# Optimization experiments

Hardware: AMD Instinct MI355X
Metric: run time of the kernel (lower is better)

The kernel has to match this reference:

```python
import jax, jax.numpy as jnp
import numpy as np
from jax import lax

B, NQ, C = 2, 1024, 2048
H, DH = 16, 128
G, CD = 4, 512          # off_grps, off_dim = C // G
LR, HR = 24, 72         # low-res grid side, high-res grid side
INTER = 64
K = LR * LR             # sampled K/V tokens (grid_size == lr_size)


def setup_inputs() -> dict:
    key = jax.random.key(0)
    ks = jax.random.split(key, 16)
    s = 0.02
    d = {}
    d['hidden_states'] = jax.random.normal(ks[0], (B, NQ, C), jnp.float32)
    d['image_hd'] = jax.random.normal(ks[1], (B, HR * HR, C), jnp.float32)
    d['wq'] = jax.random.normal(ks[2], (C, C), jnp.float32) * s
    d['wk'] = jax.random.normal(ks[3], (C, C), jnp.float32) * s
    d['wv'] = jax.random.normal(ks[4], (C, C), jnp.float32) * s
    d['wo'] = jax.random.normal(ks[5], (C, C), jnp.float32) * s
    d['conv_dw_w'] = jax.random.normal(ks[6], (CD, 1, 3, 3), jnp.float32) * s
    d['ln1_w'] = jnp.ones((CD,), jnp.float32)
    d['ln1_b'] = jnp.zeros((CD,), jnp.float32)
    d['conv_lr_proj_w'] = jax.random.normal(ks[7], (INTER, CD), jnp.float32) * s
    d['proj_int_w'] = jax.random.normal(ks[8], (INTER, CD), jnp.float32) * s
    d['proj_int_b'] = jnp.zeros((INTER,), jnp.float32)
    d['ln2_w'] = jnp.ones((INTER,), jnp.float32)
    d['ln2_b'] = jnp.zeros((INTER,), jnp.float32)
    d['conv_off_w'] = jax.random.normal(ks[9], (2, INTER), jnp.float32) * s
    d['k_hd_w'] = jax.random.normal(ks[10], (C, C), jnp.float32) * s
    d['k_hd_b'] = jnp.zeros((C,), jnp.float32)
    d['v_hd_w'] = jax.random.normal(ks[11], (C, C), jnp.float32) * s
    d['v_hd_b'] = jnp.zeros((C,), jnp.float32)
    return d


def _ln_channels(x, w, b, eps=1e-5):
    # LayerNorm2d: normalize over channel axis of [N, C, H, W]
    mu = jnp.mean(x, axis=1, keepdims=True)
    var = jnp.var(x, axis=1, keepdims=True)
    xn = (x - mu) * lax.rsqrt(var + eps)
    return xn * w[None, :, None, None] + b[None, :, None, None]


def _tokens_to_grid(x, S):
    # [B, S*S, C] -> [B*G, CD, S, S]  (group channels like einops '(b) (h w) (g c) -> (b g) c h w')
    return x.reshape(B, S, S, G, CD).transpose(0, 3, 4, 1, 2).reshape(B * G, CD, S, S)


def _bilinear_sample(img, grid):
    # img [N, C, Hh, Wh]; grid [N, K, 2] (x, y) normalized to [-1, 1], align_corners=True
    N, Cc, Hh, Wh = img.shape
    x = (grid[..., 0] + 1.0) * 0.5 * (Wh - 1)
    y = (grid[..., 1] + 1.0) * 0.5 * (Hh - 1)
    x0f, y0f = jnp.floor(x), jnp.floor(y)
    wx = (x - x0f)[:, None, :]
    wy = (y - y0f)[:, None, :]
    x0 = jnp.clip(x0f.astype(jnp.int32), 0, Wh - 1)
    x1 = jnp.clip(x0 + 1, 0, Wh - 1)
    y0 = jnp.clip(y0f.astype(jnp.int32), 0, Hh - 1)
    y1 = jnp.clip(y0 + 1, 0, Hh - 1)
    imgf = img.reshape(N, Cc, Hh * Wh)
    gather = jax.vmap(lambda im, ix: im[:, ix])  # ([C,HW],[K]) -> [C,K]
    v00 = gather(imgf, y0 * Wh + x0)
    v01 = gather(imgf, y0 * Wh + x1)
    v10 = gather(imgf, y1 * Wh + x0)
    v11 = gather(imgf, y1 * Wh + x1)
    return (v00 * (1 - wx) * (1 - wy) + v01 * wx * (1 - wy)
            + v10 * (1 - wx) * wy + v11 * wx * wy)  # [N, C, K]


def _ref_grid():
    # normalized reference points as in _grid_generate (centers / (S-1) * 2 - 1)
    yy = (jnp.linspace(0.5, LR - 0.5, LR) / (LR - 1.0)) * 2.0 - 1.0
    xx = (jnp.linspace(0.5, LR - 0.5, LR) / (LR - 1.0)) * 2.0 - 1.0
    gy, gx = jnp.meshgrid(yy, xx, indexing='ij')
    return jnp.stack([gx, gy], axis=-1).reshape(K, 2)  # (x, y)


def reference(hidden_states, image_hd, wq, wk, wv, wo, conv_dw_w, ln1_w, ln1_b,
              conv_lr_proj_w, proj_int_w, proj_int_b, ln2_w, ln2_b, conv_off_w,
              k_hd_w, k_hd_b, v_hd_w, v_hd_b):
    # ---- QKV on the full sequence ----
    q = hidden_states @ wq.T
    k_txt = hidden_states @ wk.T
    v_txt = hidden_states @ wv.T

    # ---- offset network on LR image tokens (first LR*LR tokens) ----
    lr = _tokens_to_grid(hidden_states[:, :K, :], LR)          # [B*G, CD, LR, LR]
    x = lax.conv_general_dilated(lr, conv_dw_w, (1, 1), 'SAME',
                                 feature_group_count=CD,
                                 dimension_numbers=('NCHW', 'OIHW', 'NCHW'))
    x = jax.nn.silu(x)
    x = _ln_channels(x, ln1_w, ln1_b)
    x = jnp.einsum('nchw,oc->nohw', x, conv_lr_proj_w)          # 1x1 conv -> [B*G, INTER, LR, LR]
    # intention gate from spatially pooled group features
    pooled = jnp.mean(lr, axis=(2, 3))                          # [B*G, CD]
    gate = jax.nn.sigmoid(pooled @ proj_int_w.T + proj_int_b)   # [B*G, INTER]
    x = x * gate[:, :, None, None]
    x = _ln_channels(x, ln2_w, ln2_b)
    off = jnp.einsum('nchw,oc->nohw', x, conv_off_w)            # [B*G, 2, LR, LR]
    off = off.transpose(0, 2, 3, 1).reshape(B * G, K, 2)        # (x, y)
    pos = jnp.tanh(_ref_grid()[None] + off)                     # sampling locs in [-1, 1]

    # ---- deformable gather from HD features ----
    hd = _tokens_to_grid(image_hd, HR)                          # [B*G, CD, HR, HR]
    samp = _bilinear_sample(hd, pos)                            # [B*G, CD, K]
    samp = samp.reshape(B, G, CD, K).transpose(0, 3, 1, 2).reshape(B, K, C)
    k_hd = samp @ k_hd_w.T + k_hd_b
    v_hd = samp @ v_hd_w.T + v_hd_b

    # ---- attention: causal over text tokens, HD tokens fully visible ----
    k_all = jnp.concatenate([k_txt, k_hd], axis=1)              # [B, NQ+K, C]
    v_all = jnp.concatenate([v_txt, v_hd], axis=1)
    qh = q.reshape(B, NQ, H, DH).transpose(0, 2, 1, 3)
    kh = k_all.reshape(B, NQ + K, H, DH).transpose(0, 2, 1, 3)
    vh = v_all.reshape(B, NQ + K, H, DH).transpose(0, 2, 1, 3)
    scores = jnp.einsum('bhqd,bhkd->bhqk', qh, kh) / jnp.sqrt(jnp.float32(DH))
    col = jnp.arange(NQ + K)
    row = jnp.arange(NQ)
    allow = (col[None, :] >= NQ) | (col[None, :] <= row[:, None])
    scores = jnp.where(allow[None, None], scores, jnp.float32(-1e9))
    attn = jax.nn.softmax(scores, axis=-1)
    out = jnp.einsum('bhqk,bhkd->bhqd', attn, vh)
    out = out.transpose(0, 2, 1, 3).reshape(B, NQ, C)
    return out @ wo.T
```

## Files before the change

### kernel.cpp

```cpp
#include <hip/hip_runtime.h>

typedef unsigned short u16;
typedef unsigned int u32;
typedef __attribute__((ext_vector_type(8))) short bf8;
typedef __attribute__((ext_vector_type(4))) float f4;
typedef __attribute__((ext_vector_type(4))) unsigned short us4;

constexpr int B = 2;
constexpr int NQ = 1024;
constexpr int C = 2048;
constexpr int DH = 128;
constexpr int G = 4;
constexpr int CD = 512;
constexpr int LR = 24;
constexpr int HR = 72;
constexpr int INTER = 64;
constexpr int K = LR * LR;
constexpr int NKV = NQ + K;

#define MFMA16(a, b, c) __builtin_amdgcn_mfma_f32_16x16x32_bf16(a, b, c, 0, 0, 0)
#define GLDS(g, l)                                                         \
  __builtin_amdgcn_global_load_lds(                                        \
      (const __attribute__((address_space(1))) void*)(g),                  \
      (__attribute__((address_space(3))) void*)(l), 16, 0, 0)
#define SB()                               \
  do {                                     \
    __builtin_amdgcn_sched_barrier(0);     \
    __builtin_amdgcn_s_barrier();          \
    __builtin_amdgcn_sched_barrier(0);     \
  } while (0)
#define WVM(n)                                              \
  do {                                                      \
    asm volatile("s_waitcnt vmcnt(" #n ")" ::: "memory");   \
    __builtin_amdgcn_sched_barrier(0);                      \
  } while (0)

__device__ __forceinline__ u16 f2bf1(float f) {
  u32 u = __float_as_uint(f);
  u32 r = (u + 0x7fffu + ((u >> 16) & 1u)) >> 16;
  return (u16)r;
}

__global__ __launch_bounds__(256) void f2bf_direct(
    const float* __restrict__ s0, const float* __restrict__ s1,
    const float* __restrict__ s2, const float* __restrict__ s3,
    const float* __restrict__ s4, const float* __restrict__ s5,
    const float* __restrict__ s6, const float* __restrict__ plrw,
    u16* __restrict__ d0, u16* __restrict__ d1, u16* __restrict__ d2,
    u16* __restrict__ d3, u16* __restrict__ d4, u16* __restrict__ d5,
    u16* __restrict__ d6, float* __restrict__ wt) {
  const int y = blockIdx.y;
  const int t = threadIdx.x;
  if (y == 7) {
    if (blockIdx.x >= 128) return;
    const int idx = blockIdx.x * 256 + t;
    wt[idx] = plrw[(idx & 63) * 512 + (idx >> 6)];
    return;
  }
  const float* s;
  u16* d;
  switch (y) {
    case 0: s = s0; d = d0; break;
    case 1: s = s1; d = d1; break;
    case 2: s = s2; d = d2; break;
    case 3: s = s3; d = d3; break;
    case 4: s = s4; d = d4; break;
    case 5: s = s5; d = d5; break;
    default: s = s6; d = d6; break;
  }
  const int row = t >> 2, c0 = (t & 3) * 16;
  const int fr = row >> 4, rr = row & 15;
  const int colA = c0, colB = c0 + 8;
  const int offA = (((fr * 2 + (colA >> 5)) * 4 + ((colA >> 3) & 3)) * 16 + rr) * 8;
  const int offB = (((fr * 2 + (colB >> 5)) * 4 + ((colB >> 3) & 3)) * 16 + rr) * 8;
#pragma unroll
  for (int p = 0; p < 4; ++p) {
    const int pc = blockIdx.x * 4 + p;
    const int mb = pc >> 5, kb = pc & 31;
    const float* src = s + (size_t)(mb * 64 + row) * 2048 + kb * 64 + c0;
    const float4 v0 = *(const float4*)(src);
    const float4 v1 = *(const float4*)(src + 4);
    const float4 v2 = *(const float4*)(src + 8);
    const float4 v3 = *(const float4*)(src + 12);
    u16* dp = d + (size_t)pc * 4096;
    us4 o0, o1, o2, o3;
    o0.x = f2bf1(v0.x); o0.y = f2bf1(v0.y); o0.z = f2bf1(v0.z); o0.w = f2bf1(v0.w);
    o1.x = f2bf1(v1.x); o1.y = f2bf1(v1.y); o1.z = f2bf1(v1.z); o1.w = f2bf1(v1.w);
    o2.x = f2bf1(v2.x); o2.y = f2bf1(v2.y); o2.z = f2bf1(v2.z); o2.w = f2bf1(v2.w);
    o3.x = f2bf1(v3.x); o3.y = f2bf1(v3.y); o3.z = f2bf1(v3.z); o3.w = f2bf1(v3.w);
    *(us4*)(dp + offA) = o0;
    *(us4*)(dp + offA + 4) = o1;
    *(us4*)(dp + offB) = o2;
    *(us4*)(dp + offB + 4) = o3;
  }
}

__global__ __launch_bounds__(256) void dwpool16(const float* __restrict__ hs,
                                                const float* __restrict__ cdw,
                                                float* __restrict__ x1,
                                                float* __restrict__ pooled) {
  __shared__ float SH[16 * 577];
  const int bidx = blockIdx.x;
  const int n = bidx >> 5, cg = bidx & 31;
  const int b = n >> 2, g = n & 3;
  const int c0 = cg * 16;
  const int t = threadIdx.x;
  {
    const int c = t & 15, pr = t >> 4;
    const float* src = hs + (size_t)b * 1024 * 2048 + g * 512 + c0 + c;
#pragma unroll 4
    for (int j = 0; j < 36; ++j) {
      const int p = j * 16 + pr;
      SH[c * 577 + p] = src[(size_t)p * 2048];
    }
  }
  __syncthreads();
  {
    const int c = t >> 4, seg = t & 15;
    float s = 0.f;
    for (int i = 0; i < 36; ++i) s += SH[c * 577 + seg * 36 + i];
    s += __shfl_xor(s, 1);
    s += __shfl_xor(s, 2);
    s += __shfl_xor(s, 4);
    s += __shfl_xor(s, 8);
    if (seg == 0) pooled[n * 512 + c0 + c] = s * (1.f / 576.f);
  }
  const size_t base_out = (size_t)(n * 512 + c0) * 576;
  for (int j = 0; j < 36; ++j) {
    const int idx = j * 256 + t;
    const int c = idx / 576, p = idx - c * 576;
    const int yy0 = p / 24, xx0 = p - yy0 * 24;
    const float* wp = cdw + (c0 + c) * 9;
    float s = 0.f;
#pragma unroll
    for (int dy = -1; dy <= 1; ++dy)
#pragma unroll
      for (int dx = -1; dx <= 1; ++dx) {
        const int yy = yy0 + dy, xx = xx0 + dx;
        if (yy < 0 || yy >= 24 || xx < 0 || xx >= 24) continue;
        s += SH[c * 577 + yy * 24 + xx] * wp[(dy + 1) * 3 + dx + 1];
      }
    x1[base_out + idx] = s / (1.f + expf(-s));
  }
}

__global__ __launch_bounds__(512, 2) void gemm_queue(
    const u16* __restrict__ Ast, const u16* __restrict__ Wq,
    const u16* __restrict__ Wk, const u16* __restrict__ Wv,
    const u16* __restrict__ sampst, const u16* __restrict__ khwst,
    const u16* __restrict__ vhwst, const float* __restrict__ khb,
    const float* __restrict__ vhb, u16* __restrict__ outq,
    u16* __restrict__ kg, u16* __restrict__ vg, u32* __restrict__ qctr) {
  __shared__ u16 As[2][4][4096];
  __shared__ u16 Bs[2][4][4096];
  __shared__ int s_item;
  const int tid = threadIdx.x, lane = tid & 63, w = tid >> 6;
  const int ks = lane >> 4, r = lane & 15;

  while (true) {
    __syncthreads();
    if (tid == 0) s_item = (int)atomicAdd(qctr, 1u);
    __syncthreads();
    const int item = s_item;
    if (item >= 480) break;

    if (item < 192) {
      const int wm = w >> 2, wn = w & 3;
      const int swz = (item & 7) * 24 + (item >> 3);
      const int mt = swz / 24, nt = swz % 24;
      const u16* Wst = (nt < 8) ? Wq : (nt < 16) ? Wk : Wv;
      const int nb0 = (nt & 7) * 4;
      const int mb0 = mt * 4;

#define ST_A03(bi, kt)                                                        \
  do {                                                                        \
    GLDS(Ast + ((size_t)(mb0 + 0) * 32 + (kt)) * 4096 + tid * 8,              \
         &As[bi][0][tid * 8]);                                                \
    GLDS(Ast + ((size_t)(mb0 + 2) * 32 + (kt)) * 4096 + tid * 8,              \
         &As[bi][2][tid * 8]);                                                \
  } while (0)
#define ST_A47(bi, kt)                                                        \
  do {                                                                        \
    GLDS(Ast + ((size_t)(mb0 + 1) * 32 + (kt)) * 4096 + tid * 8,              \
         &As[bi][1][tid * 8]);                                                \
    GLDS(Ast + ((size_t)(mb0 + 3) * 32 + (kt)) * 4096 + tid * 8,              \
         &As[bi][3][tid * 8]);                                                \
  } while (0)
#define ST_B01(bi, kt)                                                        \
  do {                                                                        \
    GLDS(Wst + ((size_t)(nb0 + 0) * 32 + (kt)) * 4096 + tid * 8,              \
         &Bs[bi][0][tid * 8]);                                                \
    GLDS(Wst + ((size_t)(nb0 + 1) * 32 + (kt)) * 4096 + tid * 8,              \
         &Bs[bi][1][tid * 8]);                                                \
  } while (0)
#define ST_B23(bi, kt)                                                        \
  do {                                                                        \
    GLDS(Wst + ((size_t)(nb0 + 2) * 32 + (kt)) * 4096 + tid * 8,              \
         &Bs[bi][2][tid * 8]);                                                \
    GLDS(Wst + ((size_t)(nb0 + 3) * 32 + (kt)) * 4096 + tid * 8,              \
         &Bs[bi][3][tid * 8]);                                                \
  } while (0)
#define RD_A(dst, bi, half, kc)                                               \
  _Pragma("unroll") for (int i2 = 0; i2 < 4; ++i2) dst[i2] =                  \
      *(const bf8*)(&As[bi][wm * 2 + (half)]                                  \
                       [((i2 * 2 + (kc)) * 4 + ks) * 128 + r * 8]);
#define RD_B(dst, bi, kc)                                                     \
  _Pragma("unroll") for (int j2 = 0; j2 < 4; ++j2) dst[j2] =                  \
      *(const bf8*)(&Bs[bi][wn][((j2 * 2 + (kc)) * 4 + ks) * 128 + r * 8]);
#define MM(ACC, AF, BF)                                                       \
  do {                                                                        \
    __builtin_amdgcn_s_setprio(1);                                            \
    _Pragma("unroll") for (int i3 = 0; i3 < 4; ++i3)                          \
        _Pragma("unroll") for (int j3 = 0; j3 < 4; ++j3) ACC[i3][j3] =        \
            MFMA16(AF[i3], BF[j3], ACC[i3][j3]);                              \
    __builtin_amdgcn_s_setprio(0);                                            \
  } while (0)

      f4 accA[4][4], accB[4][4];
#pragma unroll
      for (int i = 0; i < 4; ++i)
#pragma unroll
        for (int j = 0; j < 4; ++j) {
          accA[i][j] = f4{0.f, 0.f, 0.f, 0.f};
          accB[i][j] = f4{0.f, 0.f, 0.f, 0.f};
        }
      bf8 af[4], b0[4], b1[4];

      ST_A03(0, 0); ST_B01(0, 0); ST_B23(0, 0); ST_A47(0, 0);
      ST_A03(1, 1); ST_B01(1, 1);
      WVM(6);
      SB();

      for (int t = 0; t < 32; ++t) {
        const int buf = t & 1;
        RD_A(af, buf, 0, 0);
        RD_B(b0, buf, 0);
        if (t + 1 < 32) ST_B23(buf ^ 1, t + 1);
        SB();
        MM(accA, af, b0);
        SB();
        RD_A(af, buf, 0, 1);
        RD_B(b1, buf, 1);
        if (t + 1 < 32) ST_A47(buf ^ 1, t + 1);
        SB();
        MM(accA, af, b1);
        if (t + 1 < 32) { WVM(8); } else { WVM(0); }
        SB();
        RD_A(af, buf, 1, 0);
        if (t + 2 < 32) ST_A03(buf, t + 2);
        SB();
        MM(accB, af, b0);
        SB();
        RD_A(af, buf, 1, 1);
        if (t + 2 < 32) ST_B01(buf, t + 2);
        SB();
        MM(accB, af, b1);
        if (t + 2 < 32) { WVM(6); } else if (t + 1 < 32) { WVM(2); }
        SB();
      }

#define EPI(ACC, HALF)                                                        \
  _Pragma("unroll") for (int i = 0; i < 4; ++i)                               \
      _Pragma("unroll") for (int j = 0; j < 4; ++j)                           \
          _Pragma("unroll") for (int rr = 0; rr < 4; ++rr) {                  \
    const int m = mt * 256 + wm * 128 + (HALF)*64 + i * 16 + ks * 4 + rr;     \
    const int n = nt * 256 + wn * 64 + j * 16 + r;                            \
    const float v = ACC[i][j][rr];                                            \
    const int sel = n >> 11, nn = n & 2047, hh = nn >> 7, dd = nn & 127;      \
    const int bb = m >> 10, qq = m & 1023;                                    \
    const u16 bv = f2bf1(v);                                                  \
    if (sel == 0) {                                                           \
      outq[(size_t)m * 2048 + nn] = bv;                                       \
    } else if (sel == 1) {                                                    \
      kg[(((size_t)(bb * 16 + hh) * 50 + (qq >> 5)) * 16 + (dd >> 3)) * 256 + \
         (qq & 31) * 8 + (dd & 7)] = bv;                                      \
    } else {                                                                  \
      vg[((size_t)(bb * 16 + hh) * 200 + (qq >> 3)) * 1024 + dd * 8 +         \
         (qq & 7)] = bv;                                                      \
    }                                                                         \
  }
      EPI(accA, 0)
      EPI(accB, 1)
#undef EPI
    } else {
      u16* A3 = &As[0][0][0];
      u16* B3 = &Bs[0][0][0];
      const int htile = item - 192;
      const bool is_v = (htile >= 144);
      const int hb = is_v ? (htile - 144) : htile;
      const int mt = hb / 16, nt = hb % 16;
      const int ma0 = mt * 2, nb0 = nt * 2;
      const int wr = w >> 2, wc = w & 3;
      const u16* Wsrc = is_v ? vhwst : khwst;

#define HDS1(bi, kt)                                                          \
  do {                                                                        \
    const int kb_ = (kt) >> 1, kc_ = (kt) & 1;                                \
    GLDS(sampst + ((size_t)(ma0 + (w >> 2)) * 32 + kb_) * 4096 +              \
             (w & 3) * 1024 + kc_ * 512 + lane * 8,                           \
         &A3[(bi)*4096 + w * 512 + lane * 8]);                                \
    GLDS(Wsrc + ((size_t)(nb0 + (w >> 2)) * 32 + kb_) * 4096 +                \
             (w & 3) * 1024 + kc_ * 512 + lane * 8,                           \
         &B3[(bi)*4096 + w * 512 + lane * 8]);                                \
  } while (0)

      f4 acc[4][2];
#pragma unroll
      for (int i = 0; i < 4; ++i)
#pragma unroll
        for (int j = 0; j < 2; ++j) acc[i][j] = f4{0.f, 0.f, 0.f, 0.f};

      HDS1(0, 0);
      HDS1(1, 1);
      int rd = 0;
      for (int kt = 0; kt < 64; ++kt) {
        SB();
        if (kt + 2 < 64) {
          const int wb = (rd + 2 >= 3) ? rd - 1 : rd + 2;
          HDS1(wb, kt + 2);
          WVM(4);
        } else if (kt + 1 < 64) {
          WVM(2);
        } else {
          WVM(0);
        }
        SB();
        bf8 af2[4], bw[2];
#pragma unroll
        for (int i = 0; i < 4; ++i)
          af2[i] = *(const bf8*)(&A3[rd * 4096 + (wr * 4 + i) * 512 +
                                     ks * 128 + r * 8]);
#pragma unroll
        for (int j = 0; j < 2; ++j)
          bw[j] = *(const bf8*)(&B3[rd * 4096 + (wc * 2 + j) * 512 +
                                    ks * 128 + r * 8]);
        __builtin_amdgcn_s_setprio(1);
#pragma unroll
        for (int i = 0; i < 4; ++i)
#pragma unroll
          for (int j = 0; j < 2; ++j)
            acc[i][j] = MFMA16(af2[i], bw[j], acc[i][j]);
        __builtin_amdgcn_s_setprio(0);
        rd = (rd + 1 >= 3) ? 0 : rd + 1;
      }
#undef HDS1
      const int rbase = ks * 4;
      const float* bias = is_v ? vhb : khb;
#pragma unroll
      for (int i = 0; i < 4; ++i)
#pragma unroll
        for (int j = 0; j < 2; ++j) {
          const int nn = nt * 128 + (wc * 2 + j) * 16 + r;
          const int hh = nn >> 7, dd = nn & 127;
#pragma unroll
          for (int rr = 0; rr < 4; ++rr) {
            const int m = mt * 128 + wr * 64 + i * 16 + rbase + rr;
            const int bb = m / 576;
            const int kv = 1024 + (m - bb * 576);
            const u16 bv = f2bf1(acc[i][j][rr] + bias[nn]);
            if (!is_v) {
              kg[(((size_t)(bb * 16 + hh) * 50 + (kv >> 5)) * 16 + (dd >> 3)) *
                     256 +
                 (kv & 31) * 8 + (dd & 7)] = bv;
            } else {
              vg[((size_t)(bb * 16 + hh) * 200 + (kv >> 3)) * 1024 + dd * 8 +
                 (kv & 7)] = bv;
            }
          }
        }
    }
  }
}

__global__ __launch_bounds__(256) void gemm_out3(const u16* __restrict__ Ast,
                                                 const u16* __restrict__ W0,
                                                 float* __restrict__ outf) {
  __shared__ u16 As[3][4096];
  __shared__ u16 Bs[3][4096];
  const int tid = threadIdx.x, lane = tid & 63, w = tid >> 6;
  const int wr = w >> 1, wc = w & 1;
  const int ksl = lane >> 4, rl = lane & 15;
  const int xcd = blockIdx.x & 7, idx = blockIdx.x >> 3;
  const int mt = (xcd >> 2) * 8 + idx / 4;
  const int nt = (xcd & 3) * 4 + idx % 4;
  const u16* Wp = W0;
  const int ma0 = mt * 2;
  const int nb0 = nt * 2;

#define GST2(dstArr, srcBase, tb0, kt)                                     \
  do {                                                                     \
    const int kb_ = (kt) >> 1, kc_ = (kt) & 1;                             \
    _Pragma("unroll") for (int r2 = 0; r2 < 2; ++r2) {                     \
      const int run = r2 * 4 + w;                                          \
      GLDS(srcBase + ((size_t)((tb0) + (run >> 2)) * 32 + kb_) * 4096 +    \
               (run & 3) * 1024 + kc_ * 512 + lane * 8,                    \
           &dstArr[run * 512 + lane * 8]);                                 \
    }                                                                      \
  } while (0)

  f4 acc[4][4];
#pragma unroll
  for (int i = 0; i < 4; ++i)
#pragma unroll
    for (int j = 0; j < 4; ++j) acc[i][j] = f4{0.f, 0.f, 0.f, 0.f};

  GST2(As[0], Ast, ma0, 0);
  GST2(Bs[0], Wp, nb0, 0);
  GST2(As[1], Ast, ma0, 1);
  GST2(Bs[1], Wp, nb0, 1);
  int rd = 0;
  for (int kt = 0; kt < 64; ++kt) {
    SB();
    if (kt + 2 < 64) {
      const int wb = (rd + 2 >= 3) ? rd - 1 : rd + 2;
      GST2(As[wb], Ast, ma0, kt + 2);
      GST2(Bs[wb], Wp, nb0, kt + 2);
      WVM(8);
    } else if (kt + 1 < 64) {
      WVM(4);
    } else {
      WVM(0);
    }
    SB();
    bf8 af[4], bw[4];
#pragma unroll
    for (int i = 0; i < 4; ++i)
      af[i] = *(const bf8*)(&As[rd][(wr * 4 + i) * 512 + ksl * 128 + rl * 8]);
#pragma unroll
    for (int j = 0; j < 4; ++j)
      bw[j] = *(const bf8*)(&Bs[rd][(wc * 4 + j) * 512 + ksl * 128 + rl * 8]);
    __builtin_amdgcn_s_setprio(1);
#pragma unroll
    for (int i = 0; i < 4; ++i)
#pragma unroll
      for (int j = 0; j < 4; ++j)
        acc[i][j] = MFMA16(af[i], bw[j], acc[i][j]);
    __builtin_amdgcn_s_setprio(0);
    rd = (rd + 1 >= 3) ? 0 : rd + 1;
  }
#undef GST2

  const int rbase = ksl * 4;
#pragma unroll
  for (int i = 0; i < 4; ++i)
#pragma unroll
    for (int j = 0; j < 4; ++j) {
      const int n = nt * 128 + wc * 64 + j * 16 + rl;
#pragma unroll
      for (int rr = 0; rr < 4; ++rr) {
        const int m = mt * 128 + wr * 64 + i * 16 + rbase + rr;
        outf[(size_t)m * 2048 + n] = acc[i][j][rr];
      }
    }
}

__global__ __launch_bounds__(256) void lnproj_gate(
    const float* __restrict__ x1, const float* __restrict__ ln1w,
    const float* __restrict__ ln1b, const float* __restrict__ wt,
    const float* __restrict__ pooled, const float* __restrict__ piw,
    const float* __restrict__ pib, float* __restrict__ x2,
    float* __restrict__ gate) {
  __shared__ float Xs[512][68];
  __shared__ float rs[4][64], rss[4][64];
  const int bidx = blockIdx.x;
  const int t = threadIdx.x;
  if (bidx >= 72) {
    const int idx = (bidx - 72) * 256 + t;
    const int n = idx >> 6, o = idx & 63;
    const float* pb = pooled + n * 512;
    const float* wb = piw + o * 512;
    float s = pib[o];
    for (int c = 0; c < 512; ++c) s += pb[c] * wb[c];
    gate[idx] = 1.f / (1.f + expf(-s));
    return;
  }
  const int n = bidx / 9, pc = bidx % 9;
  const int p0 = pc * 64;
  {
    const int pl = t & 63, c4 = t >> 6;
    const float* src = x1 + (size_t)n * 512 * 576 + p0 + pl;
#pragma unroll 4
    for (int j = 0; j < 128; ++j) {
      const int c = j * 4 + c4;
      Xs[c][pl] = src[(size_t)c * 576];
    }
  }
  __syncthreads();
  {
    const int pl = t & 63, q = t >> 6;
    float s = 0.f, ss = 0.f;
    for (int c = q * 128; c < q * 128 + 128; ++c) {
      const float v = Xs[c][pl];
      s += v;
      ss += v * v;
    }
    rs[q][pl] = s;
    rss[q][pl] = ss;
    __syncthreads();
    const float S = rs[0][pl] + rs[1][pl] + rs[2][pl] + rs[3][pl];
    const float SS = rss[0][pl] + rss[1][pl] + rss[2][pl] + rss[3][pl];
    const float mean = S * (1.f / 512.f);
    const float inv = rsqrtf(SS * (1.f / 512.f) - mean * mean + 1e-5f);
    for (int c = q * 128; c < q * 128 + 128; ++c)
      Xs[c][pl] = (Xs[c][pl] - mean) * inv * ln1w[c] + ln1b[c];
  }
  __syncthreads();
  {
    const int o4 = (t & 15) * 4, pl0 = (t >> 4) * 4;
    float acc[4][4] = {};
    for (int c = 0; c < 512; ++c) {
      const f4 xv = *(const f4*)(&Xs[c][pl0]);
      const f4 wv = *(const f4*)(&wt[c * 64 + o4]);
#pragma unroll
      for (int i = 0; i < 4; ++i)
#pragma unroll
        for (int j = 0; j < 4; ++j) acc[i][j] += wv[i] * xv[j];
    }
#pragma unroll
    for (int i = 0; i < 4; ++i) {
      f4 ov;
      ov[0] = acc[i][0]; ov[1] = acc[i][1];
      ov[2] = acc[i][2]; ov[3] = acc[i][3];
      *(f4*)(&x2[(size_t)(n * 64 + o4 + i) * 576 + p0 + pl0]) = ov;
    }
  }
}

__global__ __launch_bounds__(256) void pos_sample(
    const float* __restrict__ x2, const float* __restrict__ gate,
    const float* __restrict__ ln2w, const float* __restrict__ ln2b,
    const float* __restrict__ offw, const float* __restrict__ img,
    u16* __restrict__ sampst) {
  const int bk = blockIdx.x;
  const int b = bk / K, k = bk % K;
  __shared__ int s_idx[G][4];
  __shared__ float s_w[G][4];
  const int t = threadIdx.x;
  const int g = t >> 6, lane = t & 63;
  {
    const int n = b * G + g;
    float v = x2[((size_t)n * INTER + lane) * K + k] * gate[n * INTER + lane];
    float s = v, ss = v * v;
    for (int o = 32; o; o >>= 1) {
      s += __shfl_xor(s, o);
      ss += __shfl_xor(ss, o);
    }
    const float mean = s * (1.f / INTER);
    const float var = ss * (1.f / INTER) - mean * mean;
    const float xn = (v - mean) * rsqrtf(var + 1e-5f) * ln2w[lane] + ln2b[lane];
    float ox = xn * offw[lane];
    float oy = xn * offw[INTER + lane];
    for (int o = 32; o; o >>= 1) {
      ox += __shfl_xor(ox, o);
      oy += __shfl_xor(oy, o);
    }
    if (lane == 0) {
      const int yi = k / LR, xi = k % LR;
      const float rx = (xi + 0.5f) / 23.f * 2.f - 1.f;
      const float ry = (yi + 0.5f) / 23.f * 2.f - 1.f;
      const float px = tanhf(rx + ox), py = tanhf(ry + oy);
      const float x = (px + 1.f) * 0.5f * (HR - 1);
      const float y = (py + 1.f) * 0.5f * (HR - 1);
      const float x0f = floorf(x), y0f = floorf(y);
      const float wx = x - x0f, wy = y - y0f;
      const int x0 = min(max((int)x0f, 0), HR - 1);
      const int x1 = min(x0 + 1, HR - 1);
      const int y0 = min(max((int)y0f, 0), HR - 1);
      const int y1 = min(y0 + 1, HR - 1);
      s_idx[g][0] = y0 * HR + x0;
      s_idx[g][1] = y0 * HR + x1;
      s_idx[g][2] = y1 * HR + x0;
      s_idx[g][3] = y1 * HR + x1;
      s_w[g][0] = (1.f - wx) * (1.f - wy);
      s_w[g][1] = wx * (1.f - wy);
      s_w[g][2] = (1.f - wx) * wy;
      s_w[g][3] = wx * wy;
    }
  }
  __syncthreads();
  const int m = b * 576 + k;
  const int mb = m >> 6, fr = (m >> 4) & 3, r = m & 15;
  const int ch0 = t * 8;
  const int gg = ch0 >> 9;
  const float* ib = img + (size_t)b * HR * HR * C + ch0;
  float v[8];
#pragma unroll
  for (int j = 0; j < 8; ++j) v[j] = 0.f;
#pragma unroll
  for (int q = 0; q < 4; ++q) {
    const float wq_ = s_w[gg][q];
    const float* p = ib + (size_t)s_idx[gg][q] * C;
    const float4 a = *(const float4*)p;
    const float4 c = *(const float4*)(p + 4);
    v[0] += wq_ * a.x; v[1] += wq_ * a.y; v[2] += wq_ * a.z; v[3] += wq_ * a.w;
    v[4] += wq_ * c.x; v[5] += wq_ * c.y; v[6] += wq_ * c.z; v[7] += wq_ * c.w;
  }
  const int kb = ch0 >> 6, kc = (ch0 >> 5) & 1, ks3 = (ch0 >> 3) & 3;
  u16* dst = sampst + ((size_t)(mb * 32 + kb)) * 4096 +
             (((fr * 2 + kc) * 4 + ks3) * 16 + r) * 8;
  us4 o0, o1;
  o0.x = f2bf1(v[0]); o0.y = f2bf1(v[1]); o0.z = f2bf1(v[2]); o0.w = f2bf1(v[3]);
  o1.x = f2bf1(v[4]); o1.y = f2bf1(v[5]); o1.z = f2bf1(v[6]); o1.w = f2bf1(v[7]);
  *(us4*)dst = o0;
  *(us4*)(dst + 4) = o1;
}

__global__ __launch_bounds__(256) void attn_u64(
    const u16* __restrict__ qb, const u16* __restrict__ kg,
    const u16* __restrict__ vg, u16* __restrict__ aob_st) {
  const int i = blockIdx.x;
  const int pair = i & 255, half = i >> 8;
  const int bh = pair & 31;
  const int q8 = pair >> 5;
  const int qblk = half ? (15 - q8) : q8;
  const int b = bh >> 4, h = bh & 15;
  const int q0 = qblk * 64;
  const int tid = threadIdx.x, lane = tid & 63, w = tid >> 6;
  const int qw = q0 + w * 16;
  const int col = lane & 15, kpart = lane >> 4, rbase = kpart * 4;
  __shared__ u16 Ks[2][8192];
  __shared__ u16 Vs[2][8192];
  __shared__ u16 Pl[4][16 * 72];
  bf8 qf[4];
  {
    const u16* qp =
        qb + (size_t)(b * 1024 + qw + col) * 2048 + h * 128 + kpart * 8;
#pragma unroll
    for (int dc = 0; dc < 4; ++dc) qf[dc] = *(const bf8*)(qp + dc * 32);
  }
  f4 o[8];
#pragma unroll
  for (int df = 0; df < 8; ++df) o[df] = f4{0.f, 0.f, 0.f, 0.f};
  float m_r[4] = {-1e30f, -1e30f, -1e30f, -1e30f};
  float l_p[4] = {0.f, 0.f, 0.f, 0.f};
  const float scale = 0.08838834764831845f;
  const int nt_text = qblk + 1;
  const int nt = nt_text + 9;
  const u16* kbh = kg + (size_t)bh * (NKV * 128);
  const u16* vbh = vg + (size_t)bh * (NKV * 128);
  u16* pw = &Pl[w][0];

#define ASTG64(bi, kv0)                                                       \
  do {                                                                        \
    const u16* gk = kbh + (size_t)((kv0) >> 5) * 4096 + w * 2048 + lane * 8;  \
    GLDS(gk, &Ks[bi][w * 2048 + lane * 8]);                                   \
    GLDS(gk + 512, &Ks[bi][w * 2048 + 512 + lane * 8]);                       \
    GLDS(gk + 1024, &Ks[bi][w * 2048 + 1024 + lane * 8]);                     \
    GLDS(gk + 1536, &Ks[bi][w * 2048 + 1536 + lane * 8]);                     \
    const u16* gv = vbh + (size_t)((kv0) >> 3) * 1024 + w * 2048 + lane * 8;  \
    GLDS(gv, &Vs[bi][w * 2048 + lane * 8]);                                   \
    GLDS(gv + 512, &Vs[bi][w * 2048 + 512 + lane * 8]);                       \
    GLDS(gv + 1024, &Vs[bi][w * 2048 + 1024 + lane * 8]);                     \
    GLDS(gv + 1536, &Vs[bi][w * 2048 + 1536 + lane * 8]);                     \
  } while (0)

  ASTG64(0, 0);
  int cur = 0;
  for (int t = 0; t < nt; ++t) {
    const bool is_text = t < nt_text;
    const int kv0 = is_text ? (t << 6) : (1024 + ((t - nt_text) << 6));
    SB();
    if (t + 1 < nt) {
      const int t1 = t + 1;
      const int kv1 =
          (t1 < nt_text) ? (t1 << 6) : (1024 + ((t1 - nt_text) << 6));
      ASTG64(cur ^ 1, kv1);
      WVM(8);
    } else {
      WVM(0);
    }
    SB();
    const u16* ksb = &Ks[cur][0];
    const u16* vsb = &Vs[cur][0];
    f4 s0 = {0.f, 0.f, 0.f, 0.f}, s1 = {0.f, 0.f, 0.f, 0.f};
    f4 s2 = {0.f, 0.f, 0.f, 0.f}, s3 = {0.f, 0.f, 0.f, 0.f};
    __builtin_amdgcn_s_setprio(1);
#pragma unroll
    for (int dc = 0; dc < 4; ++dc) {
      const int dblk = dc * 4 + kpart;
      bf8 k0f = *(const bf8*)(ksb + (dblk * 32 + col) * 8);
      bf8 k1f = *(const bf8*)(ksb + (dblk * 32 + 16 + col) * 8);
      bf8 k2f = *(const bf8*)(ksb + 4096 + (dblk * 32 + col) * 8);
      bf8 k3f = *(const bf8*)(ksb + 4096 + (dblk * 32 + 16 + col) * 8);
      s0 = MFMA16(qf[dc], k0f, s0);
      s1 = MFMA16(qf[dc], k1f, s1);
      s2 = MFMA16(qf[dc], k2f, s2);
      s3 = MFMA16(qf[dc], k3f, s3);
    }
    __builtin_amdgcn_s_setprio(0);
    float sa[4][4], loc[4], p[4][4];
    bool grow = false;
    const bool need_mask = is_text && (kv0 + 63 > qw);
#pragma unroll
    for (int rr = 0; rr < 4; ++rr) {
      float a0 = s0[rr] * scale, a1 = s1[rr] * scale;
      float a2 = s2[rr] * scale, a3 = s3[rr] * scale;
      if (need_mask) {
        const int qg = qw + rbase + rr;
        if (kv0 + col > qg) a0 = -1e30f;
        if (kv0 + 16 + col > qg) a1 = -1e30f;
        if (kv0 + 32 + col > qg) a2 = -1e30f;
        if (kv0 + 48 + col > qg) a3 = -1e30f;
      }
      sa[rr][0] = a0; sa[rr][1] = a1; sa[rr][2] = a2; sa[rr][3] = a3;
      loc[rr] = fmaxf(fmaxf(a0, a1), fmaxf(a2, a3));
      grow |= (loc[rr] > m_r[rr] + 8.f);
    }
    if (__any(grow)) {
      float fr[4];
#pragma unroll
      for (int rr = 0; rr < 4; ++rr) {
        float mx = loc[rr];
        mx = fmaxf(mx, __shfl_xor(mx, 1));
        mx = fmaxf(mx, __shfl_xor(mx, 2));
        mx = fmaxf(mx, __shfl_xor(mx, 4));
        mx = fmaxf(mx, __shfl_xor(mx, 8));
        const float mn = fmaxf(m_r[rr], mx);
        fr[rr] = __expf(m_r[rr] - mn);
        m_r[rr] = mn;
#pragma unroll
        for (int jj = 0; jj < 4; ++jj) p[rr][jj] = __expf(sa[rr][jj] - mn);
        l_p[rr] = l_p[rr] * fr[rr] + p[rr][0] + p[rr][1] + p[rr][2] + p[rr][3];
      }
#pragma unroll
      for (int df = 0; df < 8; ++df) {
        o[df][0] *= fr[0]; o[df][1] *= fr[1];
        o[df][2] *= fr[2]; o[df][3] *= fr[3];
      }
    } else {
#pragma unroll
      for (int rr = 0; rr < 4; ++rr) {
#pragma unroll
        for (int jj = 0; jj < 4; ++jj) p[rr][jj] = __expf(sa[rr][jj] - m_r[rr]);
        l_p[rr] += p[rr][0] + p[rr][1] + p[rr][2] + p[rr][3];
      }
    }
#pragma unroll
    for (int rr = 0; rr < 4; ++rr) {
      pw[(rbase + rr) * 72 + col] = f2bf1(p[rr][0]);
      pw[(rbase + rr) * 72 + 16 + col] = f2bf1(p[rr][1]);
      pw[(rbase + rr) * 72 + 32 + col] = f2bf1(p[rr][2]);
      pw[(rbase + rr) * 72 + 48 + col] = f2bf1(p[rr][3]);
    }
    bf8 pa0 = *(const bf8*)(pw + col * 72 + kpart * 8);
    bf8 pa1 = *(const bf8*)(pw + col * 72 + 32 + kpart * 8);
    __builtin_amdgcn_s_setprio(1);
#pragma unroll
    for (int df = 0; df < 8; ++df) {
      bf8 vf0 = *(const bf8*)(vsb + (kpart * 128 + df * 16 + col) * 8);
      bf8 vf1 = *(const bf8*)(vsb + ((kpart + 4) * 128 + df * 16 + col) * 8);
      o[df] = MFMA16(pa0, vf0, o[df]);
      o[df] = MFMA16(pa1, vf1, o[df]);
    }
    __builtin_amdgcn_s_setprio(0);
    cur ^= 1;
  }
#undef ASTG64
  float inv[4];
#pragma unroll
  for (int rr = 0; rr < 4; ++rr) {
    float ps = l_p[rr];
    ps += __shfl_xor(ps, 1);
    ps += __shfl_xor(ps, 2);
    ps += __shfl_xor(ps, 4);
    ps += __shfl_xor(ps, 8);
    inv[rr] = 1.f / ps;
  }
#pragma unroll
  for (int rr = 0; rr < 4; ++rr) {
    const int m = b * 1024 + qw + rbase + rr;
    const int mb = m >> 6, fr3 = (m >> 4) & 3, r16 = m & 15;
#pragma unroll
    for (int df = 0; df < 8; ++df) {
      const int ncol = h * 128 + df * 16 + col;
      const int kb = ncol >> 6, kc = (ncol >> 5) & 1, ks3 = (ncol >> 3) & 3,
                j0 = ncol & 7;
      aob_st[((size_t)(mb * 32 + kb)) * 4096 +
             (((fr3 * 2 + kc) * 4 + ks3) * 16 + r16) * 8 + j0] =
          f2bf1(o[df][rr] * inv[rr]);
    }
  }
}

extern "C" void kernel_launch(void* const* d_in, const int* in_sizes, int n_in,
                              void* d_out, int out_size, void* d_ws,
                              size_t ws_size, hipStream_t stream) {
  const float* hs = (const float*)d_in[0];
  const float* img = (const float*)d_in[1];
  const float* wq = (const float*)d_in[2];
  const float* wk = (const float*)d_in[3];
  const float* wv = (const float*)d_in[4];
  const float* wo = (const float*)d_in[5];
  const float* cdw = (const float*)d_in[6];
  const float* ln1w = (const float*)d_in[7];
  const float* ln1b = (const float*)d_in[8];
  const float* plrw = (const float*)d_in[9];
  const float* piw = (const float*)d_in[10];
  const float* pib = (const float*)d_in[11];
  const float* ln2w = (const float*)d_in[12];
  const float* ln2b = (const float*)d_in[13];
  const float* offw = (const float*)d_in[14];
  const float* khw = (const float*)d_in[15];
  const float* khb = (const float*)d_in[16];
  const float* vhw = (const float*)d_in[17];
  const float* vhb = (const float*)d_in[18];
  float* outp = (float*)d_out;

  u16* wsp = (u16*)d_ws;
  const size_t SZ = 4194304;
  u16* hs_st = wsp;
  u16* wq_st = wsp + SZ;
  u16* wk_st = wsp + 2 * SZ;
  u16* wv_st = wsp + 3 * SZ;
  u16* wo_st = wsp + 4 * SZ;
  u16* khw_st = wsp + 5 * SZ;
  u16* vhw_st = wsp + 6 * SZ;
  u16* qb_bf = wsp + 7 * SZ;
  u16* samp_st = wsp + 8 * SZ;
  u16* kg = wsp + 8 * SZ + 2359296;
  u16* vg = kg + 6553600;
  float* x1b = (float*)kg + 2359296;
  float* x2b = x1b + 2359296;
  float* poolb = x2b + 294912;
  float* gb = poolb + 4096;
  float* wtb = (float*)(vg + 6553600);
  u32* qctr = (u32*)(wtb + 32768);
  u16* aob_st = wq_st;

  dim3 blk(256);
  dwpool16<<<dim3(256), blk, 0, stream>>>(hs, cdw, x1b, poolb);
  f2bf_direct<<<dim3(256, 8), blk, 0, stream>>>(hs, wq, wk, wv, wo, khw, vhw,
                                                plrw, hs_st, wq_st, wk_st,
                                                wv_st, wo_st, khw_st, vhw_st,
                                                wtb);
  lnproj_gate<<<dim3(74), blk, 0, stream>>>(x1b, ln1w, ln1b, wtb, poolb, piw,
                                            pib, x2b, gb);
  pos_sample<<<dim3(B * K), blk, 0, stream>>>(x2b, gb, ln2w, ln2b, offw, img,
                                              samp_st);
  hipMemsetAsync(qctr, 0, 4, stream);
  gemm_queue<<<dim3(256), dim3(512), 0, stream>>>(
      hs_st, wq_st, wk_st, wv_st, samp_st, khw_st, vhw_st, khb, vhb, qb_bf,
      kg, vg, qctr);
  attn_u64<<<dim3(512), blk, 0, stream>>>(qb_bf, kg, vg, aob_st);
  gemm_out3<<<dim3(256), blk, 0, stream>>>(aob_st, wo_st, outp);
}
```

Baseline: 320.2 us.

## Split persistent work-queue GEMM into separate HD and QKV GEMM launches

Replaces the persistent atomic work-queue kernel, which mixed 192 large QKV tiles with 288 small HD K/V tiles, with two plain grid launches: one for the HD K/V projection (288 blocks) followed by one for the QKV projection (192 blocks). This drops the atomic counter, the memset and the per-item block synchronisation, and lets each kernel get its own register and LDS budget. In exchange it loses the dynamic load balancing across the two GEMMs and adds a launch boundary, so the 192-block QKV GEMM runs as a single partial wave on 256 CUs.

After: 329.2 us. 1.03x slower.

```diff
diff --git a/kernel.cpp b/kernel.cpp
--- a/kernel.cpp
+++ b/kernel.cpp
@@ -144,33 +144,21 @@
   }
 }
 
-__global__ __launch_bounds__(512, 2) void gemm_queue(
+__global__ __launch_bounds__(512, 2) void gemm256(
     const u16* __restrict__ Ast, const u16* __restrict__ Wq,
     const u16* __restrict__ Wk, const u16* __restrict__ Wv,
-    const u16* __restrict__ sampst, const u16* __restrict__ khwst,
-    const u16* __restrict__ vhwst, const float* __restrict__ khb,
-    const float* __restrict__ vhb, u16* __restrict__ outq,
-    u16* __restrict__ kg, u16* __restrict__ vg, u32* __restrict__ qctr) {
+    u16* __restrict__ outq, u16* __restrict__ kg, u16* __restrict__ vg) {
   __shared__ u16 As[2][4][4096];
   __shared__ u16 Bs[2][4][4096];
-  __shared__ int s_item;
   const int tid = threadIdx.x, lane = tid & 63, w = tid >> 6;
   const int ks = lane >> 4, r = lane & 15;
-
-  while (true) {
-    __syncthreads();
-    if (tid == 0) s_item = (int)atomicAdd(qctr, 1u);
-    __syncthreads();
-    const int item = s_item;
-    if (item >= 480) break;
-
-    if (item < 192) {
-      const int wm = w >> 2, wn = w & 3;
-      const int swz = (item & 7) * 24 + (item >> 3);
-      const int mt = swz / 24, nt = swz % 24;
-      const u16* Wst = (nt < 8) ? Wq : (nt < 16) ? Wk : Wv;
-      const int nb0 = (nt & 7) * 4;
-      const int mb0 = mt * 4;
+  const int bid = blockIdx.x;
+  const int wm = w >> 2, wn = w & 3;
+  const int swz = (bid & 7) * 24 + (bid >> 3);
+  const int mt = swz / 24, nt = swz % 24;
+  const u16* Wst = (nt < 8) ? Wq : (nt < 16) ? Wk : Wv;
+  const int nb0 = (nt & 7) * 4;
+  const int mb0 = mt * 4;
 
 #define ST_A03(bi, kt)                                                        \
   do {                                                                        \
@@ -216,48 +204,48 @@
     __builtin_amdgcn_s_setprio(0);                                            \
   } while (0)
 
-      f4 accA[4][4], accB[4][4];
-#pragma unroll
-      for (int i = 0; i < 4; ++i)
-#pragma unroll
-        for (int j = 0; j < 4; ++j) {
-          accA[i][j] = f4{0.f, 0.f, 0.f, 0.f};
-          accB[i][j] = f4{0.f, 0.f, 0.f, 0.f};
-        }
-      bf8 af[4], b0[4], b1[4];
-
-      ST_A03(0, 0); ST_B01(0, 0); ST_B23(0, 0); ST_A47(0, 0);
-      ST_A03(1, 1); ST_B01(1, 1);
-      WVM(6);
-      SB();
-
-      for (int t = 0; t < 32; ++t) {
-        const int buf = t & 1;
-        RD_A(af, buf, 0, 0);
-        RD_B(b0, buf, 0);
-        if (t + 1 < 32) ST_B23(buf ^ 1, t + 1);
-        SB();
-        MM(accA, af, b0);
-        SB();
-        RD_A(af, buf, 0, 1);
-        RD_B(b1, buf, 1);
-        if (t + 1 < 32) ST_A47(buf ^ 1, t + 1);
-        SB();
-        MM(accA, af, b1);
-        if (t + 1 < 32) { WVM(8); } else { WVM(0); }
-        SB();
-        RD_A(af, buf, 1, 0);
-        if (t + 2 < 32) ST_A03(buf, t + 2);
-        SB();
-        MM(accB, af, b0);
-        SB();
-        RD_A(af, buf, 1, 1);
-        if (t + 2 < 32) ST_B01(buf, t + 2);
-        SB();
-        MM(accB, af, b1);
-        if (t + 2 < 32) { WVM(6); } else if (t + 1 < 32) { WVM(2); }
-        SB();
-      }
+  f4 accA[4][4], accB[4][4];
+#pragma unroll
+  for (int i = 0; i < 4; ++i)
+#pragma unroll
+    for (int j = 0; j < 4; ++j) {
+      accA[i][j] = f4{0.f, 0.f, 0.f, 0.f};
+      accB[i][j] = f4{0.f, 0.f, 0.f, 0.f};
+    }
+  bf8 af[4], b0[4], b1[4];
+
+  ST_A03(0, 0); ST_B01(0, 0); ST_B23(0, 0); ST_A47(0, 0);
+  ST_A03(1, 1); ST_B01(1, 1);
+  WVM(6);
+  SB();
+
+  for (int t = 0; t < 32; ++t) {
+    const int buf = t & 1;
+    RD_A(af, buf, 0, 0);
+    RD_B(b0, buf, 0);
+    if (t + 1 < 32) ST_B23(buf ^ 1, t + 1);
+    SB();
+    MM(accA, af, b0);
+    SB();
+    RD_A(af, buf, 0, 1);
+    RD_B(b1, buf, 1);
+    if (t + 1 < 32) ST_A47(buf ^ 1, t + 1);
+    SB();
+    MM(accA, af, b1);
+    if (t + 1 < 32) { WVM(8); } else { WVM(0); }
+    SB();
+    RD_A(af, buf, 1, 0);
+    if (t + 2 < 32) ST_A03(buf, t + 2);
+    SB();
+    MM(accB, af, b0);
+    SB();
+    RD_A(af, buf, 1, 1);
+    if (t + 2 < 32) ST_B01(buf, t + 2);
+    SB();
+    MM(accB, af, b1);
+    if (t + 2 < 32) { WVM(6); } else if (t + 1 < 32) { WVM(2); }
+    SB();
+  }
 
 #define EPI(ACC, HALF)                                                        \
   _Pragma("unroll") for (int i = 0; i < 4; ++i)                               \
@@ -279,19 +267,27 @@
          (qq & 7)] = bv;                                                      \
     }                                                                         \
   }
-      EPI(accA, 0)
-      EPI(accB, 1)
+  EPI(accA, 0)
+  EPI(accB, 1)
 #undef EPI
-    } else {
-      u16* A3 = &As[0][0][0];
-      u16* B3 = &Bs[0][0][0];
-      const int htile = item - 192;
-      const bool is_v = (htile >= 144);
-      const int hb = is_v ? (htile - 144) : htile;
-      const int mt = hb / 16, nt = hb % 16;
-      const int ma0 = mt * 2, nb0 = nt * 2;
-      const int wr = w >> 2, wc = w & 3;
-      const u16* Wsrc = is_v ? vhwst : khwst;
+}
+
+__global__ __launch_bounds__(512) void gemm_hd1(
+    const u16* __restrict__ sampst, const u16* __restrict__ khwst,
+    const u16* __restrict__ vhwst, const float* __restrict__ khb,
+    const float* __restrict__ vhb, u16* __restrict__ kg,
+    u16* __restrict__ vg) {
+  __shared__ u16 A3[3 * 4096];
+  __shared__ u16 B3[3 * 4096];
+  const int tid = threadIdx.x, lane = tid & 63, w = tid >> 6;
+  const int ks = lane >> 4, r = lane & 15;
+  const int htile = blockIdx.x;
+  const bool is_v = (htile >= 144);
+  const int hb = is_v ? (htile - 144) : htile;
+  const int mt = hb / 16, nt = hb % 16;
+  const int ma0 = mt * 2, nb0 = nt * 2;
+  const int wr = w >> 2, wc = w & 3;
+  const u16* Wsrc = is_v ? vhwst : khwst;
 
 #define HDS1(bi, kt)                                                          \
   do {                                                                        \
@@ -304,72 +300,70 @@
          &B3[(bi)*4096 + w * 512 + lane * 8]);                                \
   } while (0)
 
-      f4 acc[4][2];
-#pragma unroll
-      for (int i = 0; i < 4; ++i)
-#pragma unroll
-        for (int j = 0; j < 2; ++j) acc[i][j] = f4{0.f, 0.f, 0.f, 0.f};
-
-      HDS1(0, 0);
-      HDS1(1, 1);
-      int rd = 0;
-      for (int kt = 0; kt < 64; ++kt) {
-        SB();
-        if (kt + 2 < 64) {
-          const int wb = (rd + 2 >= 3) ? rd - 1 : rd + 2;
-          HDS1(wb, kt + 2);
-          WVM(4);
-        } else if (kt + 1 < 64) {
-          WVM(2);
+  f4 acc[4][2];
+#pragma unroll
+  for (int i = 0; i < 4; ++i)
+#pragma unroll
+    for (int j = 0; j < 2; ++j) acc[i][j] = f4{0.f, 0.f, 0.f, 0.f};
+
+  HDS1(0, 0);
+  HDS1(1, 1);
+  int rd = 0;
+  for (int kt = 0; kt < 64; ++kt) {
+    SB();
+    if (kt + 2 < 64) {
+      const int wb = (rd + 2 >= 3) ? rd - 1 : rd + 2;
+      HDS1(wb, kt + 2);
+      WVM(4);
+    } else if (kt + 1 < 64) {
+      WVM(2);
+    } else {
+      WVM(0);
+    }
+    SB();
+    bf8 af2[4], bw[2];
+#pragma unroll
+    for (int i = 0; i < 4; ++i)
+      af2[i] =
+          *(const bf8*)(&A3[rd * 4096 + (wr * 4 + i) * 512 + ks * 128 + r * 8]);
+#pragma unroll
+    for (int j = 0; j < 2; ++j)
+      bw[j] =
+          *(const bf8*)(&B3[rd * 4096 + (wc * 2 + j) * 512 + ks * 128 + r * 8]);
+    __builtin_amdgcn_s_setprio(1);
+#pragma unroll
+    for (int i = 0; i < 4; ++i)
+#pragma unroll
+      for (int j = 0; j < 2; ++j)
+        acc[i][j] = MFMA16(af2[i], bw[j], acc[i][j]);
+    __builtin_amdgcn_s_setprio(0);
+    rd = (rd + 1 >= 3) ? 0 : rd + 1;
+  }
+#undef HDS1
+  const int rbase = ks * 4;
+  const float* bias = is_v ? vhb : khb;
+#pragma unroll
+  for (int i = 0; i < 4; ++i)
+#pragma unroll
+    for (int j = 0; j < 2; ++j) {
+      const int nn = nt * 128 + (wc * 2 + j) * 16 + r;
+      const int hh = nn >> 7, dd = nn & 127;
+#pragma unroll
+      for (int rr = 0; rr < 4; ++rr) {
+        const int m = mt * 128 + wr * 64 + i * 16 + rbase + rr;
+        const int bb = m / 576;
+        const int kv = 1024 + (m - bb * 576);
+        const u16 bv = f2bf1(acc[i][j][rr] + bias[nn]);
+        if (!is_v) {
+          kg[(((size_t)(bb * 16 + hh) * 50 + (kv >> 5)) * 16 + (dd >> 3)) *
+                 256 +
+             (kv & 31) * 8 + (dd & 7)] = bv;
         } else {
-          WVM(0);
+          vg[((size_t)(bb * 16 + hh) * 200 + (kv >> 3)) * 1024 + dd * 8 +
+             (kv & 7)] = bv;
         }
-        SB();
-        bf8 af2[4], bw[2];
-#pragma unroll
-        for (int i = 0; i < 4; ++i)
-          af2[i] = *(const bf8*)(&A3[rd * 4096 + (wr * 4 + i) * 512 +
-                                     ks * 128 + r * 8]);
-#pragma unroll
-        for (int j = 0; j < 2; ++j)
-          bw[j] = *(const bf8*)(&B3[rd * 4096 + (wc * 2 + j) * 512 +
-                                    ks * 128 + r * 8]);
-        __builtin_amdgcn_s_setprio(1);
-#pragma unroll
-        for (int i = 0; i < 4; ++i)
-#pragma unroll
-          for (int j = 0; j < 2; ++j)
-            acc[i][j] = MFMA16(af2[i], bw[j], acc[i][j]);
-        __builtin_amdgcn_s_setprio(0);
-        rd = (rd + 1 >= 3) ? 0 : rd + 1;
       }
-#undef HDS1
-      const int rbase = ks * 4;
-      const float* bias = is_v ? vhb : khb;
-#pragma unroll
-      for (int i = 0; i < 4; ++i)
-#pragma unroll
-        for (int j = 0; j < 2; ++j) {
-          const int nn = nt * 128 + (wc * 2 + j) * 16 + r;
-          const int hh = nn >> 7, dd = nn & 127;
-#pragma unroll
-          for (int rr = 0; rr < 4; ++rr) {
-            const int m = mt * 128 + wr * 64 + i * 16 + rbase + rr;
-            const int bb = m / 576;
-            const int kv = 1024 + (m - bb * 576);
-            const u16 bv = f2bf1(acc[i][j][rr] + bias[nn]);
-            if (!is_v) {
-              kg[(((size_t)(bb * 16 + hh) * 50 + (kv >> 5)) * 16 + (dd >> 3)) *
-                     256 +
-                 (kv & 31) * 8 + (dd & 7)] = bv;
-            } else {
-              vg[((size_t)(bb * 16 + hh) * 200 + (kv >> 3)) * 1024 + dd * 8 +
-                 (kv & 7)] = bv;
-            }
-          }
-        }
-    }
-  }
+    }
 }
 
 __global__ __launch_bounds__(256) void gemm_out3(const u16* __restrict__ Ast,
@@ -824,7 +818,6 @@
   float* poolb = x2b + 294912;
   float* gb = poolb + 4096;
   float* wtb = (float*)(vg + 6553600);
-  u32* qctr = (u32*)(wtb + 32768);
   u16* aob_st = wq_st;
 
   dim3 blk(256);
@@ -837,10 +830,10 @@
                                             pib, x2b, gb);
   pos_sample<<<dim3(B * K), blk, 0, stream>>>(x2b, gb, ln2w, ln2b, offw, img,
                                               samp_st);
-  hipMemsetAsync(qctr, 0, 4, stream);
-  gemm_queue<<<dim3(256), dim3(512), 0, stream>>>(
-      hs_st, wq_st, wk_st, wv_st, samp_st, khw_st, vhw_st, khb, vhb, qb_bf,
-      kg, vg, qctr);
+  gemm_hd1<<<dim3(288), dim3(512), 0, stream>>>(samp_st, khw_st, vhw_st, khb,
+                                                vhb, kg, vg);
+  gemm256<<<dim3(192), dim3(512), 0, stream>>>(hs_st, wq_st, wk_st, wv_st,
+                                               qb_bf, kg, vg);
   attn_u64<<<dim3(512), blk, 0, stream>>>(qb_bf, kg, vg, aob_st);
   gemm_out3<<<dim3(256), blk, 0, stream>>>(aob_st, wo_st, outp);
 }
```
